# Kernel optimization log

Hardware: AMD Instinct MI355X
Metric: run time of the kernel (lower is better)

Reference implementation:

```python
import jax, jax.numpy as jnp
import numpy as np
import math

# PIM parameters (match init_kwargs)
WL_W = 8          # weight bit width
WL_A = 8          # activation bit width
CELLBIT = 2       # bits per memristor cell
SUBARRAY = 128    # crossbar column size
ADC = 5           # ADC precision bits
ONOFF = 10.0      # on/off conductance ratio
VARI = 0.05       # state-dependent variation std
SAF_PROP = 0.001  # stuck-at-fault probability
STRIDE = 1
PAD = 1


def adc_quant(x, bit):
    # LinearQuantizeOut: uniform quantization between global min/max to 2^bit levels
    mn = jnp.min(x)
    delta = jnp.max(x) - mn
    step = delta * (2.0 ** (-bit))
    step = jnp.where(step <= 0, 1.0, step)
    idx = jnp.clip(jnp.floor((x - mn) / step), 0.0, 2.0 ** bit - 1.0)
    return idx * step + mn


def _forward(x, weight, bias):
    N, C, H, W = x.shape
    out_ch, _, kh, kw = weight.shape
    # im2col (channel-major patch ordering, same as torch.nn.Unfold)
    patches = jax.lax.conv_general_dilated_patches(
        x, (kh, kw), (STRIDE, STRIDE), ((PAD, PAD), (PAD, PAD)))  # [N, C*kh*kw, Ho, Wo]
    _, L, Ho, Wo = patches.shape
    inp = patches.reshape(N, L, Ho * Wo).transpose(0, 2, 1).reshape(-1, L)  # [rows, L]
    wflat = weight.reshape(out_ch, L)

    cellRange = 2 ** CELLBIT
    n_cells = WL_W // CELLBIT - 1   # loop count as in original (drops top cell)
    n_abits = WL_A - 1
    lower = 1.0 / ONOFF

    # activation quantization, per-tensor (qa_tensor)
    a_levels = 2.0 ** (WL_A - 1) - 1.0
    a_scale = jnp.maximum(jnp.max(inp), 1e-8) / a_levels
    inputQ = jnp.round(inp / a_scale)

    # pad columns to a multiple of SUBARRAY
    numSub = math.ceil(L / SUBARRAY)
    padn = numSub * SUBARRAY - L
    inputQ = jnp.pad(inputQ, ((0, 0), (0, padn))).reshape(-1, numSub, SUBARRAY)
    wpad = jnp.pad(wflat, ((0, 0), (0, padn))).reshape(out_ch, numSub, SUBARRAY)

    # weight quantization per (out_channel, subarray) group (qw_tensor)
    w_levels = 2.0 ** (WL_W - 1) - 1.0
    w_scale = jnp.maximum(jnp.max(jnp.abs(wpad), axis=-1, keepdims=True), 1e-8) / w_levels  # [out, numSub, 1]
    wq = jnp.round(wpad / w_scale)  # signed ints in [-w_levels, w_levels]

    # randomness: SAF masks fixed per cell level k (apply_SAF, done once);
    # state-dependent noise drawn fresh for every (z, k) iteration as in forward()
    kmask, knoise = jax.random.split(jax.random.key(42))
    probs = jax.random.uniform(kmask, (n_cells,) + wq.shape)
    sa0 = probs < SAF_PROP
    sa1 = probs > 1.0 - SAF_PROP
    noise = jax.random.normal(knoise, (n_abits, n_cells) + wq.shape) * VARI

    rows = inputQ.shape[0]
    output = jnp.zeros((rows, out_ch), dtype=x.dtype)
    ws_T = w_scale[:, :, 0].T[:, None, :]  # [numSub, 1, out]

    for z in range(n_abits):
        inputB = jnp.fmod(inputQ, 2.0)
        inputQ = jnp.round((inputQ - inputB) / 2.0)
        Xd = wq
        outD = jnp.zeros((rows, out_ch), dtype=x.dtype)
        for k in range(n_cells):
            rem = jnp.fmod(Xd, float(cellRange))
            Xd = jnp.round((Xd - rem) / cellRange)
            rQ = rem + rem * noise[z, k]          # state_dependent variation
            rQ = jnp.where(sa0[k], lower, rQ)      # stuck-at-0 -> low conductance
            rQ = jnp.where(sa1[k], jnp.sign(rQ), rQ)  # stuck-at-1 -> full conductance
            # [numSub, rows, sub] x [numSub, sub, out] -> [numSub, rows, out]
            partial = jnp.einsum('srk,sko->sro', inputB.transpose(1, 0, 2), rQ.transpose(1, 2, 0))
            pq = (adc_quant(partial, ADC) * ws_T).sum(0)  # [rows, out]
            outD = outD + pq * float(cellRange ** k)
        output = output + outD * (2.0 ** z) * a_scale

    out = output.reshape(N, Ho, Wo, out_ch).transpose(0, 3, 1, 2)
    return out + bias[None, :, None, None]


def setup_inputs() -> dict:
    key = jax.random.key(0)
    k1, k2, k3 = jax.random.split(key, 3)
    x = jax.random.uniform(k1, (8, 64, 32, 32), dtype=jnp.float32)  # post-ReLU-like activations
    weight = jax.random.normal(k2, (128, 64, 3, 3), dtype=jnp.float32) * 0.05
    bias = jax.random.normal(k3, (128,), dtype=jnp.float32) * 0.01
    return {"x": x, "weight": weight, "bias": bias}


def reference(x, weight, bias):
    return _forward(x, weight, bias)
```

## Files before the change

kernel.cpp:

```cpp
#include <hip/hip_runtime.h>
#include <stdint.h>

#define FPOFF _Pragma("clang fp contract(off)")

#define ROWS 8192
#define OC 128
#define NS 5
#define SUB 128
#define LP 640
#define LREAL 576
#define NZ 7
#define NK 3
#define NSLOT 21
#define NPTOT 245760
#define NNTOT 1720320
#define PARTSZ 5242880

#define OFF_HDR      0u
#define OFF_WSCALE   256u
#define OFF_WQ       4096u
#define OFF_CLS      86016u
#define OFF_INPUTQ   331776u
#define OFF_PACKB    5574656u
#define OFF_RQ       10162176u
#define OFF_PARTS    17043456u
#define OFF_OUTACC   142872576u

struct U2 { uint32_t x, y; };

__host__ __device__ static inline uint32_t rotl32(uint32_t v, int d){ return (v << d) | (v >> (32 - d)); }

__host__ __device__ static inline U2 threefry(uint32_t k0, uint32_t k1, uint32_t c0, uint32_t c1){
  uint32_t ks2 = k0 ^ k1 ^ 0x1BD11BDAu;
  uint32_t x0 = c0 + k0, x1 = c1 + k1;
#define TFR(r) { x0 += x1; x1 = rotl32(x1, r); x1 ^= x0; }
  TFR(13) TFR(15) TFR(26) TFR(6)  x0 += k1;  x1 += ks2 + 1u;
  TFR(17) TFR(29) TFR(16) TFR(24) x0 += ks2; x1 += k0 + 2u;
  TFR(13) TFR(15) TFR(26) TFR(6)  x0 += k0;  x1 += k1 + 3u;
  TFR(17) TFR(29) TFR(16) TFR(24) x0 += k1;  x1 += ks2 + 4u;
  TFR(13) TFR(15) TFR(26) TFR(6)  x0 += ks2; x1 += k0 + 5u;
#undef TFR
  U2 r; r.x = x0; r.y = x1; return r;
}

__device__ static inline float u2f(uint32_t b){
  return __uint_as_float((b >> 9) | 0x3F800000u) - 1.0f;
}

__device__ static inline uint32_t encf(float f){
  uint32_t u = __float_as_uint(f);
  return (u & 0x80000000u) ? ~u : (u | 0x80000000u);
}
__device__ static inline float decf(uint32_t e){
  return (e & 0x80000000u) ? __uint_as_float(e & 0x7FFFFFFFu) : __uint_as_float(~e);
}

__device__ static inline float xla_erfinv(float x){
  FPOFF
  float m = x * x;
  float w = -(float)log1p((double)(-m));
  float p;
  if (w < 5.0f){
    w = w - 2.5f;
    p = 2.81022636e-08f;
    p = 3.43273939e-07f  + p * w;
    p = -3.5233877e-06f  + p * w;
    p = -4.39150654e-06f + p * w;
    p = 0.00021858087f   + p * w;
    p = -0.00125372503f  + p * w;
    p = -0.00417768164f  + p * w;
    p = 0.246640727f     + p * w;
    p = 1.50140941f      + p * w;
  } else {
    w = (float)sqrt((double)w) - 3.0f;
    p = -0.000200214257f;
    p = 0.000100950558f  + p * w;
    p = 0.00134934322f   + p * w;
    p = -0.00367342844f  + p * w;
    p = 0.00573950773f   + p * w;
    p = -0.0076224613f   + p * w;
    p = 0.00943887047f   + p * w;
    p = 1.00167406f      + p * w;
    p = 2.83297682f      + p * w;
  }
  return p * x;
}


__global__ void k_init(uint32_t* hdr){
  int t = threadIdx.x;
  if (t == 0) hdr[0] = 0u;
  if (t < NSLOT){ hdr[8 + t] = 0xFFFFFFFFu; hdr[32 + t] = 0u; }
}

__global__ void k_xmax(const float* __restrict__ x, uint32_t* hdr){
  __shared__ float red[4];
  int t = threadIdx.x;
  const float4* x4 = (const float4*)x;
  int base = blockIdx.x * 1024 + t;
  float m = 0.0f;
#pragma unroll
  for (int i = 0; i < 4; ++i){
    float4 v = x4[base + i * 256];
    m = fmaxf(m, fmaxf(fmaxf(v.x, v.y), fmaxf(v.z, v.w)));
  }
  for (int off = 32; off; off >>= 1) m = fmaxf(m, __shfl_down(m, off));
  if ((t & 63) == 0) red[t >> 6] = m;
  __syncthreads();
  if (t == 0){
    m = fmaxf(fmaxf(red[0], red[1]), fmaxf(red[2], red[3]));
    atomicMax(&hdr[0], encf(m));
  }
}

__global__ void k_wq(const float* __restrict__ wt, float* __restrict__ wscale, int8_t* __restrict__ wq){
  FPOFF
  int s = blockIdx.x, o = blockIdx.y, t = threadIdx.x;
  int l0 = s * SUB + t, l1 = l0 + 64;
  float w0 = (l0 < LREAL) ? wt[o * LREAL + l0] : 0.f;
  float w1 = (l1 < LREAL) ? wt[o * LREAL + l1] : 0.f;
  float m = fmaxf(fabsf(w0), fabsf(w1));
  for (int off = 32; off; off >>= 1) m = fmaxf(m, __shfl_down(m, off));
  m = __shfl(m, 0);
  float ws = fmaxf(m, 1e-8f) / 127.0f;
  if (t == 0) wscale[s * OC + o] = ws;
  wq[o * LP + l0] = (int8_t)(int)rintf(w0 / ws);
  wq[o * LP + l1] = (int8_t)(int)rintf(w1 / ws);
}

__global__ void k_inputq(const float* __restrict__ x, const uint32_t* __restrict__ hdr, uint8_t* __restrict__ iq){
  FPOFF
  int r = blockIdx.x, t = threadIdx.x;
  float a_scale = fmaxf(decf(hdr[0]), 1e-8f) / 127.0f;
  int n = r >> 10, hw = r & 1023, oh = hw >> 5, ow = hw & 31;
  for (int l = t; l < LP; l += 256){
    float val = 0.f;
    if (l < LREAL){
      int c = l / 9, r9 = l - c * 9, ki = r9 / 3, kj = r9 - ki * 3;
      int ih = oh - 1 + ki, iw = ow - 1 + kj;
      if ((unsigned)ih < 32u && (unsigned)iw < 32u)
        val = x[(((n << 6) + c) << 10) + (ih << 5) + iw];
    }
    iq[r * LP + l] = (uint8_t)(int)rintf(val / a_scale);
  }
}

__global__ void k_pack(const uint8_t* __restrict__ iq, uint32_t* __restrict__ packB){
  int gid = blockIdx.x * 256 + threadIdx.x;
  if (gid >= ROWS * 20) return;
  int r = gid / 20, sw = gid - r * 20;
  const uint4* p4 = (const uint4*)(iq + r * LP + sw * 32);
  uint4 a = p4[0], b2 = p4[1];
  uint32_t wds[8] = {a.x, a.y, a.z, a.w, b2.x, b2.y, b2.z, b2.w};
  uint32_t out[NZ];
#pragma unroll
  for (int z = 0; z < NZ; ++z) out[z] = 0u;
#pragma unroll
  for (int tt = 0; tt < 32; ++tt){
    uint32_t byte = (wds[tt >> 2] >> ((tt & 3) * 8)) & 0xFFu;
#pragma unroll
    for (int z = 0; z < NZ; ++z) out[z] |= ((byte >> z) & 1u) << tt;
  }
#pragma unroll
  for (int z = 0; z < NZ; ++z) packB[(z * ROWS + r) * 20 + sw] = out[z];
}

__global__ void k_cls(uint8_t* __restrict__ cls, uint32_t km0, uint32_t km1){
  int i = blockIdx.x * 256 + threadIdx.x;
  if (i >= NPTOT) return;
  U2 r = threefry(km0, km1, 0u, (uint32_t)i);
  float f = u2f(r.x ^ r.y);
  cls[i] = (f < 0.001f) ? 1 : ((f > 0.999f) ? 2 : 0);
}

__global__ void k_rq(const int8_t* __restrict__ wq, const uint8_t* __restrict__ cls,
                     float* __restrict__ rq, uint32_t kn0, uint32_t kn1){
  FPOFF
  int i = blockIdx.x * 256 + threadIdx.x;
  if (i >= NNTOT) return;
  U2 rr = threefry(kn0, kn1, 0u, (uint32_t)i);
  uint32_t bits = rr.x ^ rr.y;
  int j = i & 127;
  int t = i >> 7;
  int s = t % 5;
  int t2 = t / 5;
  int o = t2 & 127;
  int t3 = t2 >> 7;
  int k = t3 % 3;
  int z = t3 / 3;
  float f = u2f(bits);
  float u = fmaxf(-0x1.fffffep-1f, f * 2.0f + (-0x1.fffffep-1f));
  float nv = (0x1.6a09e6p+0f * xla_erfinv(u)) * 0.05f;
  int wv = (int)wq[o * LP + s * SUB + j];
  int r0 = wv % 4;  int x1 = (wv - r0) / 4;
  int r1 = x1 % 4;  int x2 = (x1 - r1) / 4;
  int r2 = x2 % 4;
  int rem = (k == 0) ? r0 : ((k == 1) ? r1 : r2);
  float remf = (float)rem;
  float v = remf + remf * nv;
  int c = cls[((k * OC + o) * NS + s) * SUB + j];
  if (c == 1) v = 0.1f;
  else if (c == 2) v = (v > 0.f) ? 1.f : ((v < 0.f) ? -1.f : 0.f);
  rq[(((z * NK + k) * NS + s) * SUB + j) * OC + o] = v;
}

__global__ __launch_bounds__(256) void k_mmq(
    const float* __restrict__ rq_z, const uint32_t* __restrict__ packB_z,
    float* __restrict__ partCur, const float* __restrict__ partPrev,
    const float* __restrict__ wscale, uint32_t* __restrict__ hdr,
    float* __restrict__ outacc, float* __restrict__ out,
    const float* __restrict__ bias, int z)
{
  FPOFF
  const int bz = blockIdx.z;
  if (bz < 15){
    __shared__ float lrq[128 * 32];
    __shared__ float red[8];
    const int tid  = threadIdx.x;
    const int wave = tid >> 6;
    const int lane = tid & 63;
    const int k    = bz / 5;
    const int s    = bz - k * 5;
    const int slot = z * NK + k;
    const float* rq_slice = rq_z + (size_t)k * (NS * SUB * OC);
    float* partial = partCur + (size_t)k * PARTSZ;
    const int r0   = blockIdx.x * 128 + lane;
    const int OB   = blockIdx.y * 32;
    const int o0   = OB + wave * 8;

    {
      const float* gsrc = rq_slice + (size_t)s * SUB * OC + OB;
#pragma unroll
      for (int it = 0; it < 4; ++it){
        const int f = it * 256 + tid;
        const int j = f >> 3, q = f & 7;
        const float4 v = *(const float4*)(gsrc + (size_t)j * OC + q * 4);
        *(float4*)&lrq[j * 32 + q * 4] = v;
      }
    }

    const uint4 bwa4 = *(const uint4*)(packB_z + (size_t)r0 * 20 + s * 4);
    const uint4 bwb4 = *(const uint4*)(packB_z + (size_t)(r0 + 64) * 20 + s * 4);
    const uint32_t bwa[4] = {bwa4.x, bwa4.y, bwa4.z, bwa4.w};
    const uint32_t bwb[4] = {bwb4.x, bwb4.y, bwb4.z, bwb4.w};

    __syncthreads();

    float acc0[8], acc1[8];
#pragma unroll
    for (int i = 0; i < 8; ++i){ acc0[i] = 0.f; acc1[i] = 0.f; }

#pragma unroll
    for (int w = 0; w < 4; ++w){
      const uint32_t ba = bwa[w], bb = bwb[w];
#pragma unroll
      for (int jj = 0; jj < 32; ++jj){
        const int mska = ((int)(ba << (31 - jj))) >> 31;
        const int mskb = ((int)(bb << (31 - jj))) >> 31;
        const float bfa = __uint_as_float((uint32_t)mska & 0x3F800000u);
        const float bfb = __uint_as_float((uint32_t)mskb & 0x3F800000u);
        const float* lp = &lrq[(w * 32 + jj) * 32 + wave * 8];
#pragma unroll
        for (int i = 0; i < 8; ++i){
          const float rv = lp[i];
          acc0[i] = __builtin_fmaf(rv, bfa, acc0[i]);
          acc1[i] = __builtin_fmaf(rv, bfb, acc1[i]);
        }
      }
    }

    {
      float4* p0 = (float4*)(partial + (size_t)(s * ROWS + r0) * OC + o0);
      p0[0] = make_float4(acc0[0], acc0[1], acc0[2], acc0[3]);
      p0[1] = make_float4(acc0[4], acc0[5], acc0[6], acc0[7]);
      float4* p1 = (float4*)(partial + (size_t)(s * ROWS + r0 + 64) * OC + o0);
      p1[0] = make_float4(acc1[0], acc1[1], acc1[2], acc1[3]);
      p1[1] = make_float4(acc1[4], acc1[5], acc1[6], acc1[7]);
    }

    float mn = acc0[0], mx = acc0[0];
#pragma unroll
    for (int i = 1; i < 8; ++i){ mn = fminf(mn, acc0[i]); mx = fmaxf(mx, acc0[i]); }
#pragma unroll
    for (int i = 0; i < 8; ++i){ mn = fminf(mn, acc1[i]); mx = fmaxf(mx, acc1[i]); }
    for (int off = 32; off; off >>= 1){
      mn = fminf(mn, __shfl_down(mn, off));
      mx = fmaxf(mx, __shfl_down(mx, off));
    }
    if (lane == 0){ red[wave] = mn; red[4 + wave] = mx; }
    __syncthreads();
    if (tid == 0){
      mn = fminf(fminf(red[0], red[1]), fminf(red[2], red[3]));
      mx = fmaxf(fmaxf(red[4], red[5]), fmaxf(red[6], red[7]));
      atomicMin(&hdr[8 + slot], encf(mn));
      atomicMax(&hdr[32 + slot], encf(mx));
    }
  } else {
    const int zP = z - 1;
    const int qid = (bz - 15) * 256 + blockIdx.y * 64 + blockIdx.x;
    const int e = qid * 256 + threadIdx.x;
    const int r = e >> 7, o = e & 127;
    float pqk[NK];
#pragma unroll
    for (int k = 0; k < NK; ++k){
      const float* part = partPrev + (size_t)k * PARTSZ;
      float mn = decf(hdr[8 + zP * NK + k]);
      float mx = decf(hdr[32 + zP * NK + k]);
      float step = (mx - mn) * 0.03125f;
      if (!(step > 0.f)) step = 1.0f;
      float pq = 0.f;
#pragma unroll
      for (int s = 0; s < NS; ++s){
        float v = part[(size_t)(s * ROWS + r) * OC + o];
        float fidx = floorf((v - mn) / step);
        fidx = fminf(fmaxf(fidx, 0.f), 31.f);
        float qv = fidx * step + mn;
        pq = pq + qv * wscale[s * OC + o];
      }
      pqk[k] = pq;
    }
    float outD = pqk[0] + pqk[1] * 4.0f;
    float tt = outD + pqk[2] * 16.0f;
    float a_scale = fmaxf(decf(hdr[0]), 1e-8f) / 127.0f;
    float contrib = (tt * (float)(1 << zP)) * a_scale;
    if (zP == 0) outacc[e] = contrib;
    else outacc[e] = outacc[e] + contrib;
  }
}

__global__ void k_quantz(const float* __restrict__ p0, const float* __restrict__ p1,
                         const float* __restrict__ p2, const float* __restrict__ wscale,
                         const uint32_t* __restrict__ hdr, float* __restrict__ outacc,
                         float* __restrict__ out, const float* __restrict__ bias, int z){
  FPOFF
  int e = blockIdx.x * 256 + threadIdx.x;
  int r = e >> 7, o = e & 127;
  float pqk[NK];
#pragma unroll
  for (int k = 0; k < NK; ++k){
    const float* part = (k == 0) ? p0 : ((k == 1) ? p1 : p2);
    float mn = decf(hdr[8 + z * NK + k]);
    float mx = decf(hdr[32 + z * NK + k]);
    float step = (mx - mn) * 0.03125f;
    if (!(step > 0.f)) step = 1.0f;
    float pq = 0.f;
#pragma unroll
    for (int s = 0; s < NS; ++s){
      float v = part[(size_t)(s * ROWS + r) * OC + o];
      float fidx = floorf((v - mn) / step);
      fidx = fminf(fmaxf(fidx, 0.f), 31.f);
      float qv = fidx * step + mn;
      pq = pq + qv * wscale[s * OC + o];
    }
    pqk[k] = pq;
  }
  float outD = pqk[0] + pqk[1] * 4.0f;
  float tt = outD + pqk[2] * 16.0f;
  float a_scale = fmaxf(decf(hdr[0]), 1e-8f) / 127.0f;
  float contrib = (tt * (float)(1 << z)) * a_scale;
  if (z == 0) outacc[e] = contrib;
  else if (z < NZ - 1) outacc[e] = outacc[e] + contrib;
  else {
    float res = outacc[e] + contrib;
    int n = r >> 10, hw = r & 1023;
    out[(((n << 7) + o) << 10) + hw] = res + bias[o];
  }
}

extern "C" void kernel_launch(void* const* d_in, const int* in_sizes, int n_in,
                              void* d_out, int out_size, void* d_ws, size_t ws_size,
                              hipStream_t stream){
  const float* x    = (const float*)d_in[0];
  const float* wt   = (const float*)d_in[1];
  const float* bias = (const float*)d_in[2];
  float* out = (float*)d_out;
  char* ws = (char*)d_ws;
  uint32_t* hdr    = (uint32_t*)(ws + OFF_HDR);
  float*    wscale = (float*)(ws + OFF_WSCALE);
  int8_t*   wq     = (int8_t*)(ws + OFF_WQ);
  uint8_t*  cls    = (uint8_t*)(ws + OFF_CLS);
  uint8_t*  iq     = (uint8_t*)(ws + OFF_INPUTQ);
  uint32_t* packB  = (uint32_t*)(ws + OFF_PACKB);
  float*    rq     = (float*)(ws + OFF_RQ);
  float*    parts  = (float*)(ws + OFF_PARTS);
  float*    outacc = (float*)(ws + OFF_OUTACC);

  U2 p0 = threefry(0u, 42u, 0u, 0u);
  U2 p1 = threefry(0u, 42u, 0u, 1u);
  uint32_t km0 = p0.x, km1 = p0.y, kn0 = p1.x, kn1 = p1.y;

  hipLaunchKernelGGL(k_init,   dim3(1),           dim3(64),  0, stream, hdr);
  hipLaunchKernelGGL(k_xmax,   dim3(128),         dim3(256), 0, stream, x, hdr);
  hipLaunchKernelGGL(k_wq,     dim3(5, 128),      dim3(64),  0, stream, wt, wscale, wq);
  hipLaunchKernelGGL(k_inputq, dim3(8192),        dim3(256), 0, stream, x, hdr, iq);
  hipLaunchKernelGGL(k_pack,   dim3(640),         dim3(256), 0, stream, iq, packB);
  hipLaunchKernelGGL(k_cls,    dim3(NPTOT / 256), dim3(256), 0, stream, cls, km0, km1);
  hipLaunchKernelGGL(k_rq,     dim3(NNTOT / 256), dim3(256), 0, stream, wq, cls, rq, kn0, kn1);

  for (int z = 0; z < NZ; ++z){
    float*       cur  = parts + (size_t)((z & 1) ? 3 : 0) * PARTSZ;
    const float* prev = parts + (size_t)((z & 1) ? 0 : 3) * PARTSZ;
    const float* rqz  = rq + (size_t)z * NK * NS * SUB * OC;
    const uint32_t* pbz = packB + (size_t)z * ROWS * 20;
    dim3 grid(64, 4, (z == 0) ? 15 : 31);
    hipLaunchKernelGGL(k_mmq, grid, dim3(256), 0, stream,
                       rqz, pbz, cur, prev, wscale, hdr, outacc, out, bias, z);
  }
  hipLaunchKernelGGL(k_quantz, dim3(4096), dim3(256), 0, stream,
                     parts, parts + PARTSZ, parts + 2 * (size_t)PARTSZ,
                     wscale, hdr, outacc, out, bias, 6);
}
```

Measured before the change: 593.1 us.

## Fuse three cell-level slices into one block sharing the bit-mask decode

Each matmul block now handles all three cell levels k for one subarray instead of a single k. The packed input bits are loaded and decoded into masks once and applied to three staged rq slices, so the bit extraction and packB loads are shared. The cost is three times the LDS per block (48KB), triple the accumulator registers, and a third as many matmul blocks. That may lower occupancy and parallelism; the quantize blocks of the previous z are renumbered to match.

```diff
diff --git a/kernel.cpp b/kernel.cpp
--- a/kernel.cpp
+++ b/kernel.cpp
@@ -213,29 +213,26 @@
 {
   FPOFF
   const int bz = blockIdx.z;
-  if (bz < 15){
-    __shared__ float lrq[128 * 32];
-    __shared__ float red[8];
+  if (bz < 5){
+    __shared__ float lrq[3 * 128 * 32];
+    __shared__ float red[24];
     const int tid  = threadIdx.x;
     const int wave = tid >> 6;
     const int lane = tid & 63;
-    const int k    = bz / 5;
-    const int s    = bz - k * 5;
-    const int slot = z * NK + k;
-    const float* rq_slice = rq_z + (size_t)k * (NS * SUB * OC);
-    float* partial = partCur + (size_t)k * PARTSZ;
+    const int s    = bz;
     const int r0   = blockIdx.x * 128 + lane;
     const int OB   = blockIdx.y * 32;
     const int o0   = OB + wave * 8;
 
-    {
-      const float* gsrc = rq_slice + (size_t)s * SUB * OC + OB;
+#pragma unroll
+    for (int kk = 0; kk < NK; ++kk){
+      const float* gsrc = rq_z + ((size_t)kk * NS + s) * (SUB * OC) + OB;
 #pragma unroll
       for (int it = 0; it < 4; ++it){
         const int f = it * 256 + tid;
         const int j = f >> 3, q = f & 7;
         const float4 v = *(const float4*)(gsrc + (size_t)j * OC + q * 4);
-        *(float4*)&lrq[j * 32 + q * 4] = v;
+        *(float4*)&lrq[kk * 4096 + j * 32 + q * 4] = v;
       }
     }
 
@@ -246,9 +243,11 @@
 
     __syncthreads();
 
-    float acc0[8], acc1[8];
-#pragma unroll
-    for (int i = 0; i < 8; ++i){ acc0[i] = 0.f; acc1[i] = 0.f; }
+    float acc0[NK][8], acc1[NK][8];
+#pragma unroll
+    for (int kk = 0; kk < NK; ++kk)
+#pragma unroll
+      for (int i = 0; i < 8; ++i){ acc0[kk][i] = 0.f; acc1[kk][i] = 0.f; }
 
 #pragma unroll
     for (int w = 0; w < 4; ++w){
@@ -259,45 +258,61 @@
         const int mskb = ((int)(bb << (31 - jj))) >> 31;
         const float bfa = __uint_as_float((uint32_t)mska & 0x3F800000u);
         const float bfb = __uint_as_float((uint32_t)mskb & 0x3F800000u);
-        const float* lp = &lrq[(w * 32 + jj) * 32 + wave * 8];
-#pragma unroll
-        for (int i = 0; i < 8; ++i){
-          const float rv = lp[i];
-          acc0[i] = __builtin_fmaf(rv, bfa, acc0[i]);
-          acc1[i] = __builtin_fmaf(rv, bfb, acc1[i]);
+        const int jb = (w * 32 + jj) * 32 + wave * 8;
+#pragma unroll
+        for (int kk = 0; kk < NK; ++kk){
+          const float* lp = &lrq[kk * 4096 + jb];
+#pragma unroll
+          for (int i = 0; i < 8; ++i){
+            const float rv = lp[i];
+            acc0[kk][i] = __builtin_fmaf(rv, bfa, acc0[kk][i]);
+            acc1[kk][i] = __builtin_fmaf(rv, bfb, acc1[kk][i]);
+          }
         }
       }
     }
 
-    {
+#pragma unroll
+    for (int kk = 0; kk < NK; ++kk){
+      float* partial = partCur + (size_t)kk * PARTSZ;
       float4* p0 = (float4*)(partial + (size_t)(s * ROWS + r0) * OC + o0);
-      p0[0] = make_float4(acc0[0], acc0[1], acc0[2], acc0[3]);
-      p0[1] = make_float4(acc0[4], acc0[5], acc0[6], acc0[7]);
+      p0[0] = make_float4(acc0[kk][0], acc0[kk][1], acc0[kk][2], acc0[kk][3]);
+      p0[1] = make_float4(acc0[kk][4], acc0[kk][5], acc0[kk][6], acc0[kk][7]);
       float4* p1 = (float4*)(partial + (size_t)(s * ROWS + r0 + 64) * OC + o0);
-      p1[0] = make_float4(acc1[0], acc1[1], acc1[2], acc1[3]);
-      p1[1] = make_float4(acc1[4], acc1[5], acc1[6], acc1[7]);
-    }
-
-    float mn = acc0[0], mx = acc0[0];
-#pragma unroll
-    for (int i = 1; i < 8; ++i){ mn = fminf(mn, acc0[i]); mx = fmaxf(mx, acc0[i]); }
-#pragma unroll
-    for (int i = 0; i < 8; ++i){ mn = fminf(mn, acc1[i]); mx = fmaxf(mx, acc1[i]); }
-    for (int off = 32; off; off >>= 1){
-      mn = fminf(mn, __shfl_down(mn, off));
-      mx = fmaxf(mx, __shfl_down(mx, off));
-    }
-    if (lane == 0){ red[wave] = mn; red[4 + wave] = mx; }
+      p1[0] = make_float4(acc1[kk][0], acc1[kk][1], acc1[kk][2], acc1[kk][3]);
+      p1[1] = make_float4(acc1[kk][4], acc1[kk][5], acc1[kk][6], acc1[kk][7]);
+    }
+
+#pragma unroll
+    for (int kk = 0; kk < NK; ++kk){
+      float mn = acc0[kk][0], mx = acc0[kk][0];
+#pragma unroll
+      for (int i = 1; i < 8; ++i){ mn = fminf(mn, acc0[kk][i]); mx = fmaxf(mx, acc0[kk][i]); }
+#pragma unroll
+      for (int i = 0; i < 8; ++i){ mn = fminf(mn, acc1[kk][i]); mx = fmaxf(mx, acc1[kk][i]); }
+      for (int off = 32; off; off >>= 1){
+        mn = fminf(mn, __shfl_down(mn, off));
+        mx = fmaxf(mx, __shfl_down(mx, off));
+      }
+      if (lane == 0){ red[wave * 6 + kk * 2] = mn; red[wave * 6 + kk * 2 + 1] = mx; }
+    }
     __syncthreads();
     if (tid == 0){
-      mn = fminf(fminf(red[0], red[1]), fminf(red[2], red[3]));
-      mx = fmaxf(fmaxf(red[4], red[5]), fmaxf(red[6], red[7]));
-      atomicMin(&hdr[8 + slot], encf(mn));
-      atomicMax(&hdr[32 + slot], encf(mx));
+#pragma unroll
+      for (int kk = 0; kk < NK; ++kk){
+        float mn = red[kk * 2], mx = red[kk * 2 + 1];
+#pragma unroll
+        for (int wv = 1; wv < 4; ++wv){
+          mn = fminf(mn, red[wv * 6 + kk * 2]);
+          mx = fmaxf(mx, red[wv * 6 + kk * 2 + 1]);
+        }
+        atomicMin(&hdr[8 + z * NK + kk], encf(mn));
+        atomicMax(&hdr[32 + z * NK + kk], encf(mx));
+      }
     }
   } else {
     const int zP = z - 1;
-    const int qid = (bz - 15) * 256 + blockIdx.y * 64 + blockIdx.x;
+    const int qid = (bz - 5) * 256 + blockIdx.y * 64 + blockIdx.x;
     const int e = qid * 256 + threadIdx.x;
     const int r = e >> 7, o = e & 127;
     float pqk[NK];
@@ -402,7 +417,7 @@
     const float* prev = parts + (size_t)((z & 1) ? 0 : 3) * PARTSZ;
     const float* rqz  = rq + (size_t)z * NK * NS * SUB * OC;
     const uint32_t* pbz = packB + (size_t)z * ROWS * 20;
-    dim3 grid(64, 4, (z == 0) ? 15 : 31);
+    dim3 grid(64, 4, (z == 0) ? 5 : 21);
     hipLaunchKernelGGL(k_mmq, grid, dim3(256), 0, stream,
                        rqz, pbz, cur, prev, wscale, hdr, outacc, out, bias, z);
   }
```

Measured after the change: 749.0 us. 26.3% more time.
